# Optimization experiments

Hardware: AMD Instinct MI355X
Metric: run time of the kernel (lower is better)

Reference implementation:

```python
import jax, jax.numpy as jnp
import numpy as np

# ---- quantization constants (8-bit, per-tensor affine; representative values) ----
Q_MAX = 255.0
S_IN, Z_IN = 0.05, 128.0      # block input
S1, Z1 = 0.04, 128.0          # after expand 1x1 + hardswish
S2, Z2 = 0.04, 128.0          # after depthwise 5x5 + hardswish
S_SE1, Z_SE1 = 0.03, 128.0    # SE fc1 output
S_SE2, Z_SE2 = 1.0 / 255.0, 0.0  # SE fc2 hardsigmoid output in [0,1]
S_MUL, Z_MUL = 0.04, 128.0    # SE gated activation
S3, Z3 = 0.05, 128.0          # after project 1x1
S_OUT, Z_OUT = 0.06, 128.0    # after residual add
W_SCALE = 0.01                # symmetric per-tensor weight scale (zero_point = 0)
EXP_C = 576                   # expanded channels (depthwise groups)


def conv(x, w, stride=1, padding=0, groups=1):
    return jax.lax.conv_general_dilated(
        x, w, (stride, stride), [(padding, padding), (padding, padding)],
        feature_group_count=groups, dimension_numbers=('NCHW', 'OIHW', 'NCHW'))


def hardswish(x):
    return x * jnp.clip(x + 3.0, 0.0, 6.0) * (1.0 / 6.0)


def hardsigmoid(x):
    return jnp.clip(x + 3.0, 0.0, 6.0) * (1.0 / 6.0)


def qconv(x_q, w_q, b_q, s_in, z_in, s_out, z_out, stride=1, padding=0, groups=1, act=None):
    """Quantized conv: int-domain accumulation (simulated in fp32), fused activation
    on the dequantized accumulator, then requantize to [0, Q_MAX]."""
    acc = conv(x_q - z_in, w_q, stride, padding, groups) + b_q[None, :, None, None]
    deq = acc * (s_in * W_SCALE)  # dequantize accumulator
    if act == 'hardswish':
        deq = hardswish(deq)
    elif act == 'hardsigmoid':
        deq = hardsigmoid(deq)
    return jnp.clip(deq * (1.0 / s_out) + z_out, 0.0, Q_MAX)


def setup_inputs() -> dict:
    key = jax.random.key(0)
    ks = jax.random.split(key, 11)
    def qw(k, shape):  # int8-style symmetric weights stored as fp32 integers
        return jnp.round(jnp.clip(jax.random.normal(k, shape) * 40.0, -127.0, 127.0))
    def qb(k, n):      # int32-style bias in accumulator domain
        return jnp.round(jax.random.normal(k, (n,)) * 500.0)
    return {
        'x':      jnp.round(jax.random.uniform(ks[0], (64, 96, 28, 28)) * Q_MAX),
        'w_exp':  qw(ks[1], (576, 96, 1, 1)),  'b_exp':  qb(ks[2], 576),
        'w_dw':   qw(ks[3], (576, 1, 5, 5)),   'b_dw':   qb(ks[4], 576),
        'w_se1':  qw(ks[5], (144, 576, 1, 1)), 'b_se1':  qb(ks[6], 144),
        'w_se2':  qw(ks[7], (576, 144, 1, 1)), 'b_se2':  qb(ks[8], 576),
        'w_proj': qw(ks[9], (96, 576, 1, 1)),  'b_proj': qb(ks[10], 96),
    }


def reference(x, w_exp, b_exp, w_dw, b_dw, w_se1, b_se1, w_se2, b_se2, w_proj, b_proj):
    # expand 1x1 (+ hardswish)
    e = qconv(x, w_exp, b_exp, S_IN, Z_IN, S1, Z1, act='hardswish')
    # depthwise 5x5, padding=(5-1)//2=2, groups=expanded (+ hardswish)
    d = qconv(e, w_dw, b_dw, S1, Z1, S2, Z2, padding=2, groups=EXP_C, act='hardswish')
    # squeeze-excitation: global avg pool -> fc1 -> fc2(hardsigmoid) -> quantized mul
    pooled = jnp.mean(d, axis=(2, 3), keepdims=True)  # [N, 576, 1, 1]
    g1 = qconv(pooled, w_se1, b_se1, S2, Z2, S_SE1, Z_SE1)
    g2 = qconv(g1, w_se2, b_se2, S_SE1, Z_SE1, S_SE2, Z_SE2, act='hardsigmoid')
    gated = jnp.clip((g2 - Z_SE2) * (d - Z2) * (S_SE2 * S2 / S_MUL) + Z_MUL, 0.0, Q_MAX)
    # project 1x1 (linear)
    p = qconv(gated, w_proj, b_proj, S_MUL, Z_MUL, S3, Z3)
    # quantized residual add (stride=1, in==out channels -> use_res_connect)
    out = jnp.clip((x - Z_IN) * (S_IN / S_OUT) + (p - Z3) * (S3 / S_OUT) + Z_OUT, 0.0, Q_MAX)
    return out
```

## Files before the change

kernel.cpp:

```cpp
#include <hip/hip_runtime.h>

typedef _Float16 v8h __attribute__((ext_vector_type(8)));
typedef _Float16 v4h __attribute__((ext_vector_type(4)));
typedef _Float16 v2h __attribute__((ext_vector_type(2)));
typedef float v4f __attribute__((ext_vector_type(4)));

#define NB 64
#define CI 96
#define CE 576
#define CO 96
#define HW 784
#define SEC 144

#if defined(__has_builtin)
#if __has_builtin(__builtin_amdgcn_fdot2)
#define HAVE_FDOT2 1
#endif
#endif

__device__ __forceinline__ float fdot2(v2h a, v2h b, float c) {
#ifdef HAVE_FDOT2
  return __builtin_amdgcn_fdot2(a, b, c, false);
#else
  return (float)a[0] * (float)b[0] + ((float)a[1] * (float)b[1] + c);
#endif
}

__global__ __launch_bounds__(256) void k0_cvt_w(const float* __restrict__ w_exp,
                                                const float* __restrict__ w_proj,
                                                _Float16* __restrict__ w_exp_h,
                                                _Float16* __restrict__ w_proj_h) {
  int i = blockIdx.x * 256 + threadIdx.x;
  if (i < CE * CI) {
    w_exp_h[i]  = (_Float16)w_exp[i];
    w_proj_h[i] = (_Float16)w_proj[i];
  }
}

__global__ __launch_bounds__(256) void k0x_pack(const float* __restrict__ x,
                                                _Float16* __restrict__ x_f) {
  __shared__ _Float16 xl[112][104];
  const int tid = threadIdx.x;
  const int n = blockIdx.y;
  const int hw0 = blockIdx.x * 112;

  for (int idx = tid; idx < CI * 28; idx += 256) {
    int c = idx / 28, seg = idx % 28;
    const float4 v = *(const float4*)&x[(n * CI + c) * HW + hw0 + seg * 4];
    int row = seg * 4;
    xl[row + 0][c] = (_Float16)(v.x - 128.0f);
    xl[row + 1][c] = (_Float16)(v.y - 128.0f);
    xl[row + 2][c] = (_Float16)(v.z - 128.0f);
    xl[row + 3][c] = (_Float16)(v.w - 128.0f);
  }
  __syncthreads();

  for (int idx = tid; idx < 1344; idx += 256) {
    int t_l = idx / 192, rem = idx % 192, s = rem / 64, ln = rem % 64;
    int hw_l = t_l * 16 + (ln & 15), ci = s * 32 + (ln >> 4) * 8;
    v8h o;
#pragma unroll
    for (int j = 0; j < 8; ++j) o[j] = xl[hw_l][ci + j];
    size_t t = (size_t)(blockIdx.x * 7 + t_l);
    *(v8h*)&x_f[(((size_t)n * 49 + t) * 3 + s) * 512 + ln * 8] = o;
  }
}

__global__ __launch_bounds__(512, 8) void k12_fused(const _Float16* __restrict__ x_f,
                                                    const _Float16* __restrict__ w_exp_h,
                                                    const float* __restrict__ b_exp,
                                                    const float* __restrict__ w_dw,
                                                    const float* __restrict__ b_dw,
                                                    _Float16* __restrict__ d_t,
                                                    float* __restrict__ d_sums2) {
  __shared__ _Float16 e_lds[16][18][38];
  __shared__ _Float16 d_tile[16][392];
  __shared__ _Float16 w_pairs[16][5][8];
  const int tid = threadIdx.x;
  const int n = blockIdx.z;
  const int h = blockIdx.y;
  const int c0 = blockIdx.x * 16;

  {
    unsigned long long* z = (unsigned long long*)&e_lds[0][0][0];
    for (int idx = tid; idx < 16 * 18 * 38 * 2 / 8; idx += 512) z[idx] = 0ull;
  }
  for (int idx = tid; idx < 640; idx += 512) {
    int c = idx / 40, r = idx % 40, dy = r / 8, k = r % 8;
    int tap = (k < 4) ? k : (k - 3);
    w_pairs[c][dy][k] = (_Float16)w_dw[(c0 + c) * 25 + dy * 5 + tap];
  }
  __syncthreads();

  const int wv = tid >> 6, lane = tid & 63;
  const int l15 = lane & 15, q = lane >> 4;

  {
    const _Float16* wrow = &w_exp_h[(c0 + l15) * CI + q * 8];
    v8h a0 = *(const v8h*)(wrow);
    v8h a1 = *(const v8h*)(wrow + 32);
    v8h a2 = *(const v8h*)(wrow + 64);
    float bia[4];
#pragma unroll
    for (int r = 0; r < 4; ++r) bia[r] = b_exp[c0 + q * 4 + r];

    const int ir0 = 14 * h - 2;
    const _Float16* xb = x_f + (size_t)n * (49 * 3 * 512) + lane * 8;
    for (int t_l = wv; t_l < 28; t_l += 8) {
      int t = 21 * h + t_l;
      const _Float16* xt = xb + (size_t)t * (3 * 512);
      v8h b0 = *(const v8h*)(xt);
      v8h b1 = *(const v8h*)(xt + 512);
      v8h b2 = *(const v8h*)(xt + 1024);
      v4f acc = (v4f){0.f, 0.f, 0.f, 0.f};
      acc = __builtin_amdgcn_mfma_f32_16x16x32_f16(a0, b0, acc, 0, 0, 0);
      acc = __builtin_amdgcn_mfma_f32_16x16x32_f16(a1, b1, acc, 0, 0, 0);
      acc = __builtin_amdgcn_mfma_f32_16x16x32_f16(a2, b2, acc, 0, 0, 0);
      int hw = t * 16 + l15;
      int y = hw / 28, xx = hw - y * 28;
      int r_l = y - ir0;
#pragma unroll
      for (int r = 0; r < 4; ++r) {
        float deq = (acc[r] + bia[r]) * 5.0e-4f;
        float cl  = fminf(fmaxf(deq + 3.0f, 0.0f), 6.0f);
        float ev  = fminf(fmaxf(deq * cl * (25.0f / 6.0f), -128.0f), 127.0f);
        e_lds[q * 4 + r][r_l][6 + xx] = (_Float16)ev;
      }
    }
  }
  __syncthreads();

  const int c = tid >> 5, l = tid & 31;
  v2h W01[5], W23[5], W12[5], W34[5];
  float W0s[5], W4s[5];
#pragma unroll
  for (int dy = 0; dy < 5; ++dy) {
    W01[dy] = *(const v2h*)&w_pairs[c][dy][0];
    W23[dy] = *(const v2h*)&w_pairs[c][dy][2];
    W12[dy] = *(const v2h*)&w_pairs[c][dy][4];
    W34[dy] = *(const v2h*)&w_pairs[c][dy][6];
    W0s[dy] = (float)W01[dy][0];
    W4s[dy] = (float)W34[dy][1];
  }
  const float bc = b_dw[c0 + c];

  float csum = 0.0f;
  if (l < 28) {
    const int ry = l >> 1;
    const int bx = (l & 1) * 14;
    v2h P0[5], P1[5], P2[5], P3[5];
#pragma unroll
    for (int dy = 0; dy < 5; ++dy) {
      const _Float16* row = &e_lds[c][ry + dy][bx];
      P0[dy] = *(const v2h*)(row + 4);
      P1[dy] = *(const v2h*)(row + 6);
      P2[dy] = *(const v2h*)(row + 8);
      P3[dy] = *(const v2h*)(row + 10);
    }
#pragma unroll
    for (int xi = 0; xi < 3; ++xi) {
      const int x0 = bx + xi * 4;
      float o0 = bc, o1 = bc, o2 = bc, o3 = bc;
#pragma unroll
      for (int dy = 0; dy < 5; ++dy) {
        o0 = fdot2(P0[dy], W01[dy], o0);
        o0 = fdot2(P1[dy], W23[dy], o0);
        o0 += (float)P2[dy][0] * W4s[dy];
        o1 += (float)P0[dy][1] * W0s[dy];
        o1 = fdot2(P1[dy], W12[dy], o1);
        o1 = fdot2(P2[dy], W34[dy], o1);
        o2 = fdot2(P1[dy], W01[dy], o2);
        o2 = fdot2(P2[dy], W23[dy], o2);
        o2 += (float)P3[dy][0] * W4s[dy];
        o3 += (float)P1[dy][1] * W0s[dy];
        o3 = fdot2(P2[dy], W12[dy], o3);
        o3 = fdot2(P3[dy], W34[dy], o3);
      }
      float oo[4] = {o0, o1, o2, o3};
      v2h dva, dvb;
#pragma unroll
      for (int i = 0; i < 4; ++i) {
        float deq = oo[i] * 4.0e-4f;
        float cl  = fminf(fmaxf(deq + 3.0f, 0.0f), 6.0f);
        float dvv = fminf(fmaxf(deq * cl * (25.0f / 6.0f), -128.0f), 127.0f);
        if (i < 2) dva[i] = (_Float16)dvv; else dvb[i - 2] = (_Float16)dvv;
        csum += dvv;
      }
      *(v2h*)&d_tile[c][ry * 28 + x0]     = dva;
      *(v2h*)&d_tile[c][ry * 28 + x0 + 2] = dvb;
#pragma unroll
      for (int dy = 0; dy < 5; ++dy) {
        const _Float16* row = &e_lds[c][ry + dy][bx];
        P0[dy] = P2[dy];
        P1[dy] = P3[dy];
        P2[dy] = *(const v2h*)(row + x0 - bx + 12);
        P3[dy] = *(const v2h*)(row + x0 - bx + 14);
      }
    }
    {
      float o0 = bc, o1 = bc;
#pragma unroll
      for (int dy = 0; dy < 5; ++dy) {
        o0 = fdot2(P0[dy], W01[dy], o0);
        o0 = fdot2(P1[dy], W23[dy], o0);
        o0 += (float)P2[dy][0] * W4s[dy];
        o1 += (float)P0[dy][1] * W0s[dy];
        o1 = fdot2(P1[dy], W12[dy], o1);
        o1 = fdot2(P2[dy], W34[dy], o1);
      }
      v2h dv;
      float oo[2] = {o0, o1};
#pragma unroll
      for (int i = 0; i < 2; ++i) {
        float deq = oo[i] * 4.0e-4f;
        float cl  = fminf(fmaxf(deq + 3.0f, 0.0f), 6.0f);
        float dvv = fminf(fmaxf(deq * cl * (25.0f / 6.0f), -128.0f), 127.0f);
        dv[i] = (_Float16)dvv;
        csum += dvv;
      }
      *(v2h*)&d_tile[c][ry * 28 + bx + 12] = dv;
    }
  }
#pragma unroll
  for (int m = 16; m >= 1; m >>= 1) csum += __shfl_xor(csum, m);
  if (l == 0) d_sums2[((size_t)h * NB + n) * CE + c0 + c] = csum;

  __syncthreads();
  const size_t obase = ((size_t)n * 72 + (c0 >> 3)) * 784 + 392 * h;
  if (tid < 392) {
    int hw_l = tid;
    v8h o0, o1;
#pragma unroll
    for (int j = 0; j < 8; ++j) { o0[j] = d_tile[j][hw_l]; o1[j] = d_tile[8 + j][hw_l]; }
    *(v8h*)&d_t[(obase + hw_l) * 8] = o0;
    *(v8h*)&d_t[(obase + 784 + hw_l) * 8] = o1;
  }
}

__global__ __launch_bounds__(256) void k3a_fc1(const float* __restrict__ d_sums2,
                                               const float* __restrict__ w_se1,
                                               const float* __restrict__ b_se1,
                                               float* __restrict__ g1) {
  const int tid = threadIdx.x;
  const int wv = tid >> 6, lane = tid & 63;
  const int n = blockIdx.y;
  const int o = blockIdx.x * 4 + wv;
  const float* wrow = &w_se1[o * CE];
  const float* s0 = &d_sums2[(size_t)n * CE];
  const float* s1 = &d_sums2[((size_t)NB + n) * CE];
  float p = 0.f;
#pragma unroll
  for (int s = 0; s < 9; ++s) {
    int cc = lane + s * 64;
    p += wrow[cc] * (s0[cc] + s1[cc]);
  }
#pragma unroll
  for (int m = 32; m >= 1; m >>= 1) p += __shfl_xor(p, m);
  if (lane == 0) {
    float deq = (p * (1.0f / 784.0f) + b_se1[o]) * 4.0e-4f;
    g1[n * SEC + o] = fminf(fmaxf(deq * 33.3333333f + 128.0f, 0.0f), 255.0f) - 128.0f;
  }
}

__global__ __launch_bounds__(256) void k3b_fc2(const float* __restrict__ g1,
                                               const float* __restrict__ w_se2,
                                               const float* __restrict__ b_se2,
                                               _Float16* __restrict__ g2h) {
  const int tid = threadIdx.x;
  const int wv = tid >> 6, lane = tid & 63;
  const int n = blockIdx.y;
  const int o = blockIdx.x * 4 + wv;
  const float* wrow = &w_se2[o * SEC];
  const float* grow = &g1[n * SEC];
  float p = wrow[lane] * grow[lane] + wrow[lane + 64] * grow[lane + 64];
  if (lane < 16) p += wrow[lane + 128] * grow[lane + 128];
#pragma unroll
  for (int m = 32; m >= 1; m >>= 1) p += __shfl_xor(p, m);
  if (lane == 0) {
    float deq = (p + b_se2[o]) * 3.0e-4f;
    g2h[n * CE + o] =
        (_Float16)(fminf(fmaxf(deq + 3.0f, 0.0f), 6.0f) * (1.0f / 6.0f));
  }
}

__global__ __launch_bounds__(192) void k4_proj(const _Float16* __restrict__ d_t,
                                               const _Float16* __restrict__ g2h,
                                               const _Float16* __restrict__ w_proj_h,
                                               const float* __restrict__ b_proj,
                                               const float* __restrict__ x,
                                               float* __restrict__ out) {
  const int tid = threadIdx.x;
  const int n = blockIdx.z;
  const int co0 = blockIdx.y * 48;
  const int hw0 = blockIdx.x * 112;
  const int wv = tid >> 6, lane = tid & 63;
  const int l15 = lane & 15, q = lane >> 4;

  v4f acc[7];
#pragma unroll
  for (int t = 0; t < 7; ++t) acc[t] = (v4f){0.f, 0.f, 0.f, 0.f};

  const _Float16* dbase = d_t + (((size_t)n * 72 + q) * 784 + hw0 + l15) * 8;
  const _Float16* abase = &w_proj_h[(co0 + wv * 16 + l15) * CE + q * 8];
  const _Float16* gbase = &g2h[(size_t)n * CE + q * 8];

  for (int ks = 0; ks < 18; ++ks) {
    v8h a = *(const v8h*)(abase + ks * 32);
    v8h g = *(const v8h*)(gbase + ks * 32);
    v8h ag = a * g;
    const _Float16* dk = dbase + (size_t)ks * (4 * 784 * 8);
#pragma unroll
    for (int t = 0; t < 7; ++t) {
      v8h b = *(const v8h*)(dk + t * (16 * 8));
      acc[t] = __builtin_amdgcn_mfma_f32_16x16x32_f16(ag, b, acc[t], 0, 0, 0);
    }
  }

  float bia[4];
#pragma unroll
  for (int r = 0; r < 4; ++r) bia[r] = b_proj[co0 + wv * 16 + q * 4 + r];

#pragma unroll
  for (int t = 0; t < 7; ++t) {
#pragma unroll
    for (int r = 0; r < 4; ++r) {
      int co = co0 + wv * 16 + q * 4 + r;
      int hw = hw0 + t * 16 + l15;
      float p = fminf(fmaxf((acc[t][r] + bia[r]) * 4.0e-4f * 20.0f + 128.0f, 0.0f), 255.0f);
      float xv = x[(n * CO + co) * HW + hw];
      float o = (xv - 128.0f) * 0.8333333333f + (p - 128.0f) * 0.8333333333f + 128.0f;
      out[(n * CO + co) * HW + hw] = fminf(fmaxf(o, 0.0f), 255.0f);
    }
  }
}

extern "C" void kernel_launch(void* const* d_in, const int* in_sizes, int n_in,
                              void* d_out, int out_size, void* d_ws, size_t ws_size,
                              hipStream_t stream) {
  const float* x      = (const float*)d_in[0];
  const float* w_exp  = (const float*)d_in[1];
  const float* b_exp  = (const float*)d_in[2];
  const float* w_dw   = (const float*)d_in[3];
  const float* b_dw   = (const float*)d_in[4];
  const float* w_se1  = (const float*)d_in[5];
  const float* b_se1  = (const float*)d_in[6];
  const float* w_se2  = (const float*)d_in[7];
  const float* b_se2  = (const float*)d_in[8];
  const float* w_proj = (const float*)d_in[9];
  const float* b_proj = (const float*)d_in[10];
  float* out = (float*)d_out;

  char* ws = (char*)d_ws;
  const size_t SZ_W  = (size_t)CE * CI * 2;
  const size_t SZ_XF = (size_t)NB * 49 * 3 * 512 * 2;
  const size_t SZ_D  = (size_t)NB * CE * HW * 2;
  const size_t SZ_S2 = (size_t)2 * NB * CE * 4;
  const size_t SZ_S  = (size_t)NB * CE * 4;
  _Float16* w_exp_h  = (_Float16*)(ws);
  _Float16* w_proj_h = (_Float16*)(ws + SZ_W);
  _Float16* x_f      = (_Float16*)(ws + 2 * SZ_W);
  _Float16* d_t      = (_Float16*)(ws + 2 * SZ_W + SZ_XF);
  float*    d_sums2  = (float*)   (ws + 2 * SZ_W + SZ_XF + SZ_D);
  float*    g1       = (float*)   (ws + 2 * SZ_W + SZ_XF + SZ_D + SZ_S2);
  _Float16* g2h      = (_Float16*)(ws + 2 * SZ_W + SZ_XF + SZ_D + SZ_S2 + SZ_S);

  k0_cvt_w<<<(CE * CI + 255) / 256, 256, 0, stream>>>(w_exp, w_proj, w_exp_h, w_proj_h);
  k0x_pack<<<dim3(7, NB), 256, 0, stream>>>(x, x_f);
  k12_fused<<<dim3(36, 2, NB), 512, 0, stream>>>(x_f, w_exp_h, b_exp, w_dw, b_dw, d_t, d_sums2);
  k3a_fc1<<<dim3(36, NB), 256, 0, stream>>>(d_sums2, w_se1, b_se1, g1);
  k3b_fc2<<<dim3(144, NB), 256, 0, stream>>>(g1, w_se2, b_se2, g2h);
  k4_proj<<<dim3(7, 2, NB), 192, 0, stream>>>(d_t, g2h, w_proj_h, b_proj, x, out);
}
```

Before: 177.6 us.

## Merge prep and SE kernels, fold requant constants into FMAs and med3 clamps

```diff
diff --git a/kernel.cpp b/kernel.cpp
--- a/kernel.cpp
+++ b/kernel.cpp
@@ -26,21 +26,35 @@
 #endif
 }
 
-__global__ __launch_bounds__(256) void k0_cvt_w(const float* __restrict__ w_exp,
-                                                const float* __restrict__ w_proj,
-                                                _Float16* __restrict__ w_exp_h,
-                                                _Float16* __restrict__ w_proj_h) {
-  int i = blockIdx.x * 256 + threadIdx.x;
-  if (i < CE * CI) {
-    w_exp_h[i]  = (_Float16)w_exp[i];
-    w_proj_h[i] = (_Float16)w_proj[i];
-  }
-}
-
-__global__ __launch_bounds__(256) void k0x_pack(const float* __restrict__ x,
-                                                _Float16* __restrict__ x_f) {
+__device__ __forceinline__ float clampf(float x, float lo, float hi) {
+#if defined(__has_builtin)
+#if __has_builtin(__builtin_amdgcn_fmed3f)
+  return __builtin_amdgcn_fmed3f(x, lo, hi);
+#else
+  return fminf(fmaxf(x, lo), hi);
+#endif
+#else
+  return fminf(fmaxf(x, lo), hi);
+#endif
+}
+
+__global__ __launch_bounds__(256) void k0_pack_cvt(const float* __restrict__ x,
+                                                   _Float16* __restrict__ x_f,
+                                                   const float* __restrict__ w_exp,
+                                                   const float* __restrict__ w_proj,
+                                                   _Float16* __restrict__ w_exp_h,
+                                                   _Float16* __restrict__ w_proj_h) {
   __shared__ _Float16 xl[112][104];
   const int tid = threadIdx.x;
+
+  if (blockIdx.y == NB) {
+    for (int i = blockIdx.x * 256 + tid; i < CE * CI; i += 7 * 256) {
+      w_exp_h[i]  = (_Float16)w_exp[i];
+      w_proj_h[i] = (_Float16)w_proj[i];
+    }
+    return;
+  }
+
   const int n = blockIdx.y;
   const int hw0 = blockIdx.x * 112;
 
@@ -100,32 +114,44 @@
     v8h a0 = *(const v8h*)(wrow);
     v8h a1 = *(const v8h*)(wrow + 32);
     v8h a2 = *(const v8h*)(wrow + 64);
-    float bia[4];
-#pragma unroll
-    for (int r = 0; r < 4; ++r) bia[r] = b_exp[c0 + q * 4 + r];
+    float bia3[4], bia2[4];
+#pragma unroll
+    for (int r = 0; r < 4; ++r) {
+      float b = b_exp[c0 + q * 4 + r];
+      bia3[r] = fmaf(b, 5.0e-4f, 3.0f);
+      bia2[r] = b * (5.0e-4f * 25.0f / 6.0f);
+    }
 
     const int ir0 = 14 * h - 2;
     const _Float16* xb = x_f + (size_t)n * (49 * 3 * 512) + lane * 8;
-    for (int t_l = wv; t_l < 28; t_l += 8) {
-      int t = 21 * h + t_l;
-      const _Float16* xt = xb + (size_t)t * (3 * 512);
-      v8h b0 = *(const v8h*)(xt);
-      v8h b1 = *(const v8h*)(xt + 512);
-      v8h b2 = *(const v8h*)(xt + 1024);
-      v4f acc = (v4f){0.f, 0.f, 0.f, 0.f};
-      acc = __builtin_amdgcn_mfma_f32_16x16x32_f16(a0, b0, acc, 0, 0, 0);
-      acc = __builtin_amdgcn_mfma_f32_16x16x32_f16(a1, b1, acc, 0, 0, 0);
-      acc = __builtin_amdgcn_mfma_f32_16x16x32_f16(a2, b2, acc, 0, 0, 0);
-      int hw = t * 16 + l15;
-      int y = hw / 28, xx = hw - y * 28;
-      int r_l = y - ir0;
-#pragma unroll
-      for (int r = 0; r < 4; ++r) {
-        float deq = (acc[r] + bia[r]) * 5.0e-4f;
-        float cl  = fminf(fmaxf(deq + 3.0f, 0.0f), 6.0f);
-        float ev  = fminf(fmaxf(deq * cl * (25.0f / 6.0f), -128.0f), 127.0f);
-        e_lds[q * 4 + r][r_l][6 + xx] = (_Float16)ev;
+    int hw0 = (21 * h + wv) * 16 + l15;
+    int y = hw0 / 28;
+    int xx = hw0 - y * 28;
+#pragma unroll
+    for (int it = 0; it < 4; ++it) {
+      int t_l = wv + it * 8;
+      if (t_l < 28) {
+        int t = 21 * h + t_l;
+        const _Float16* xt = xb + (size_t)t * (3 * 512);
+        v8h b0 = *(const v8h*)(xt);
+        v8h b1 = *(const v8h*)(xt + 512);
+        v8h b2 = *(const v8h*)(xt + 1024);
+        v4f acc = (v4f){0.f, 0.f, 0.f, 0.f};
+        acc = __builtin_amdgcn_mfma_f32_16x16x32_f16(a0, b0, acc, 0, 0, 0);
+        acc = __builtin_amdgcn_mfma_f32_16x16x32_f16(a1, b1, acc, 0, 0, 0);
+        acc = __builtin_amdgcn_mfma_f32_16x16x32_f16(a2, b2, acc, 0, 0, 0);
+        _Float16* dst = &e_lds[q * 4][y - ir0][6 + xx];
+#pragma unroll
+        for (int r = 0; r < 4; ++r) {
+          float t1  = fmaf(acc[r], 5.0e-4f, bia3[r]);
+          float cl  = clampf(t1, 0.0f, 6.0f);
+          float a2v = fmaf(acc[r], 5.0e-4f * 25.0f / 6.0f, bia2[r]);
+          float ev  = clampf(a2v * cl, -128.0f, 127.0f);
+          dst[r * (18 * 38)] = (_Float16)ev;
+        }
       }
+      xx += 16; y += 4;
+      if (xx >= 28) { xx -= 28; ++y; }
     }
   }
   __syncthreads();
@@ -143,6 +169,13 @@
     W4s[dy] = (float)W34[dy][1];
   }
   const float bc = b_dw[c0 + c];
+
+#define DW_REQUANT(oo, dvv)                                                   \
+  {                                                                           \
+    float t1_ = fmaf((oo), 4.0e-4f, 3.0f);                                    \
+    float cl_ = clampf(t1_, 0.0f, 6.0f);                                      \
+    dvv = clampf((oo) * (4.0e-4f * 25.0f / 6.0f) * cl_, -128.0f, 127.0f);     \
+  }
 
   float csum = 0.0f;
   if (l < 28) {
@@ -176,16 +209,13 @@
         o3 = fdot2(P2[dy], W12[dy], o3);
         o3 = fdot2(P3[dy], W34[dy], o3);
       }
-      float oo[4] = {o0, o1, o2, o3};
+      float d0, d1, d2, d3;
+      DW_REQUANT(o0, d0); DW_REQUANT(o1, d1);
+      DW_REQUANT(o2, d2); DW_REQUANT(o3, d3);
+      csum += (d0 + d1) + (d2 + d3);
       v2h dva, dvb;
-#pragma unroll
-      for (int i = 0; i < 4; ++i) {
-        float deq = oo[i] * 4.0e-4f;
-        float cl  = fminf(fmaxf(deq + 3.0f, 0.0f), 6.0f);
-        float dvv = fminf(fmaxf(deq * cl * (25.0f / 6.0f), -128.0f), 127.0f);
-        if (i < 2) dva[i] = (_Float16)dvv; else dvb[i - 2] = (_Float16)dvv;
-        csum += dvv;
-      }
+      dva[0] = (_Float16)d0; dva[1] = (_Float16)d1;
+      dvb[0] = (_Float16)d2; dvb[1] = (_Float16)d3;
       *(v2h*)&d_tile[c][ry * 28 + x0]     = dva;
       *(v2h*)&d_tile[c][ry * 28 + x0 + 2] = dvb;
 #pragma unroll
@@ -208,16 +238,10 @@
         o1 = fdot2(P1[dy], W12[dy], o1);
         o1 = fdot2(P2[dy], W34[dy], o1);
       }
-      v2h dv;
-      float oo[2] = {o0, o1};
-#pragma unroll
-      for (int i = 0; i < 2; ++i) {
-        float deq = oo[i] * 4.0e-4f;
-        float cl  = fminf(fmaxf(deq + 3.0f, 0.0f), 6.0f);
-        float dvv = fminf(fmaxf(deq * cl * (25.0f / 6.0f), -128.0f), 127.0f);
-        dv[i] = (_Float16)dvv;
-        csum += dvv;
-      }
+      float d0, d1;
+      DW_REQUANT(o0, d0); DW_REQUANT(o1, d1);
+      csum += d0 + d1;
+      v2h dv; dv[0] = (_Float16)d0; dv[1] = (_Float16)d1;
       *(v2h*)&d_tile[c][ry * 28 + bx + 12] = dv;
     }
   }
@@ -237,49 +261,73 @@
   }
 }
 
-__global__ __launch_bounds__(256) void k3a_fc1(const float* __restrict__ d_sums2,
-                                               const float* __restrict__ w_se1,
-                                               const float* __restrict__ b_se1,
-                                               float* __restrict__ g1) {
+__global__ __launch_bounds__(256) void k3_se(const float* __restrict__ d_sums2,
+                                             const float* __restrict__ w_se1,
+                                             const float* __restrict__ b_se1,
+                                             const float* __restrict__ w_se2,
+                                             const float* __restrict__ b_se2,
+                                             _Float16* __restrict__ g2h) {
+  __shared__ float g1s[SEC];
   const int tid = threadIdx.x;
   const int wv = tid >> 6, lane = tid & 63;
-  const int n = blockIdx.y;
-  const int o = blockIdx.x * 4 + wv;
-  const float* wrow = &w_se1[o * CE];
+  const int n = blockIdx.x;
+
+  float sreg[9];
   const float* s0 = &d_sums2[(size_t)n * CE];
   const float* s1 = &d_sums2[((size_t)NB + n) * CE];
-  float p = 0.f;
 #pragma unroll
   for (int s = 0; s < 9; ++s) {
-    int cc = lane + s * 64;
-    p += wrow[cc] * (s0[cc] + s1[cc]);
-  }
-#pragma unroll
-  for (int m = 32; m >= 1; m >>= 1) p += __shfl_xor(p, m);
-  if (lane == 0) {
-    float deq = (p * (1.0f / 784.0f) + b_se1[o]) * 4.0e-4f;
-    g1[n * SEC + o] = fminf(fmaxf(deq * 33.3333333f + 128.0f, 0.0f), 255.0f) - 128.0f;
-  }
-}
-
-__global__ __launch_bounds__(256) void k3b_fc2(const float* __restrict__ g1,
-                                               const float* __restrict__ w_se2,
-                                               const float* __restrict__ b_se2,
-                                               _Float16* __restrict__ g2h) {
-  const int tid = threadIdx.x;
-  const int wv = tid >> 6, lane = tid & 63;
-  const int n = blockIdx.y;
-  const int o = blockIdx.x * 4 + wv;
-  const float* wrow = &w_se2[o * SEC];
-  const float* grow = &g1[n * SEC];
-  float p = wrow[lane] * grow[lane] + wrow[lane + 64] * grow[lane + 64];
-  if (lane < 16) p += wrow[lane + 128] * grow[lane + 128];
-#pragma unroll
-  for (int m = 32; m >= 1; m >>= 1) p += __shfl_xor(p, m);
-  if (lane == 0) {
-    float deq = (p + b_se2[o]) * 3.0e-4f;
-    g2h[n * CE + o] =
-        (_Float16)(fminf(fmaxf(deq + 3.0f, 0.0f), 6.0f) * (1.0f / 6.0f));
+    int cc = lane + 64 * s;
+    sreg[s] = (s0[cc] + s1[cc]) * (1.0f / 784.0f);
+  }
+
+  for (int i = 0; i < 36; i += 2) {
+    const int oa = wv * 36 + i, ob = oa + 1;
+    const float* wa = &w_se1[(size_t)oa * CE];
+    const float* wb = &w_se1[(size_t)ob * CE];
+    float pa = 0.f, pb = 0.f;
+#pragma unroll
+    for (int s = 0; s < 9; ++s) {
+      pa = fmaf(wa[lane + 64 * s], sreg[s], pa);
+      pb = fmaf(wb[lane + 64 * s], sreg[s], pb);
+    }
+#pragma unroll
+    for (int m = 32; m >= 1; m >>= 1) {
+      pa += __shfl_xor(pa, m);
+      pb += __shfl_xor(pb, m);
+    }
+    if (lane == 0) {
+      g1s[oa] = clampf(fmaf(pa, 1.0f / 75.0f, fmaf(b_se1[oa], 1.0f / 75.0f, 128.0f)),
+                       0.0f, 255.0f) - 128.0f;
+      g1s[ob] = clampf(fmaf(pb, 1.0f / 75.0f, fmaf(b_se1[ob], 1.0f / 75.0f, 128.0f)),
+                       0.0f, 255.0f) - 128.0f;
+    }
+  }
+  __syncthreads();
+
+  const float g0   = g1s[lane];
+  const float g64  = g1s[lane + 64];
+  const float g128 = (lane < 16) ? g1s[lane + 128] : 0.0f;
+
+  for (int i = 0; i < 144; i += 2) {
+    const int oa = wv * 144 + i, ob = oa + 1;
+    const float* wa = &w_se2[(size_t)oa * SEC];
+    const float* wb = &w_se2[(size_t)ob * SEC];
+    float w2a = (lane < 16) ? wa[lane + 128] : 0.0f;
+    float w2b = (lane < 16) ? wb[lane + 128] : 0.0f;
+    float pa = fmaf(wa[lane], g0, fmaf(wa[lane + 64], g64, w2a * g128));
+    float pb = fmaf(wb[lane], g0, fmaf(wb[lane + 64], g64, w2b * g128));
+#pragma unroll
+    for (int m = 32; m >= 1; m >>= 1) {
+      pa += __shfl_xor(pa, m);
+      pb += __shfl_xor(pb, m);
+    }
+    if (lane == 0) {
+      float ta = fmaf(pa, 3.0e-4f, fmaf(b_se2[oa], 3.0e-4f, 3.0f));
+      float tb = fmaf(pb, 3.0e-4f, fmaf(b_se2[ob], 3.0e-4f, 3.0f));
+      g2h[(size_t)n * CE + oa] = (_Float16)(clampf(ta, 0.0f, 6.0f) * (1.0f / 6.0f));
+      g2h[(size_t)n * CE + ob] = (_Float16)(clampf(tb, 0.0f, 6.0f) * (1.0f / 6.0f));
+    }
   }
 }
 
@@ -316,9 +364,10 @@
     }
   }
 
-  float bia[4];
-#pragma unroll
-  for (int r = 0; r < 4; ++r) bia[r] = b_proj[co0 + wv * 16 + q * 4 + r];
+  float biaf[4];
+#pragma unroll
+  for (int r = 0; r < 4; ++r)
+    biaf[r] = fmaf(b_proj[co0 + wv * 16 + q * 4 + r], 8.0e-3f, 128.0f);
 
 #pragma unroll
   for (int t = 0; t < 7; ++t) {
@@ -326,10 +375,10 @@
     for (int r = 0; r < 4; ++r) {
       int co = co0 + wv * 16 + q * 4 + r;
       int hw = hw0 + t * 16 + l15;
-      float p = fminf(fmaxf((acc[t][r] + bia[r]) * 4.0e-4f * 20.0f + 128.0f, 0.0f), 255.0f);
+      float p  = clampf(fmaf(acc[t][r], 8.0e-3f, biaf[r]), 0.0f, 255.0f);
       float xv = x[(n * CO + co) * HW + hw];
-      float o = (xv - 128.0f) * 0.8333333333f + (p - 128.0f) * 0.8333333333f + 128.0f;
-      out[(n * CO + co) * HW + hw] = fminf(fmaxf(o, 0.0f), 255.0f);
+      float o = fmaf(xv + p, 0.8333333333f, -85.33333333f);
+      out[(n * CO + co) * HW + hw] = clampf(o, 0.0f, 255.0f);
     }
   }
 }
@@ -361,13 +410,10 @@
   _Float16* x_f      = (_Float16*)(ws + 2 * SZ_W);
   _Float16* d_t      = (_Float16*)(ws + 2 * SZ_W + SZ_XF);
   float*    d_sums2  = (float*)   (ws + 2 * SZ_W + SZ_XF + SZ_D);
-  float*    g1       = (float*)   (ws + 2 * SZ_W + SZ_XF + SZ_D + SZ_S2);
   _Float16* g2h      = (_Float16*)(ws + 2 * SZ_W + SZ_XF + SZ_D + SZ_S2 + SZ_S);
 
-  k0_cvt_w<<<(CE * CI + 255) / 256, 256, 0, stream>>>(w_exp, w_proj, w_exp_h, w_proj_h);
-  k0x_pack<<<dim3(7, NB), 256, 0, stream>>>(x, x_f);
+  k0_pack_cvt<<<dim3(7, NB + 1), 256, 0, stream>>>(x, x_f, w_exp, w_proj, w_exp_h, w_proj_h);
   k12_fused<<<dim3(36, 2, NB), 512, 0, stream>>>(x_f, w_exp_h, b_exp, w_dw, b_dw, d_t, d_sums2);
-  k3a_fc1<<<dim3(36, NB), 256, 0, stream>>>(d_sums2, w_se1, b_se1, g1);
-  k3b_fc2<<<dim3(144, NB), 256, 0, stream>>>(g1, w_se2, b_se2, g2h);
+  k3_se<<<dim3(NB), 256, 0, stream>>>(d_sums2, w_se1, b_se1, w_se2, b_se2, g2h);
   k4_proj<<<dim3(7, 2, NB), 192, 0, stream>>>(d_t, g2h, w_proj_h, b_proj, x, out);
 }
```

Result: slower. 225.6 us (+27.0%).
